# Kernel tuning notes

Measured on AMD Instinct MI355X. Metric: run time of the kernel, lower is better.

The kernel has to match this reference:

```python
import jax, jax.numpy as jnp
import numpy as np

N_NODES = 100000
N_EDGES = 1600000
DIMS = [21, 32, 64, 128, 21]  # conv1..conv4 (conv4 in-dim fixed to 128; source's 100 is a bug)


def _glorot(key, fan_in, fan_out):
    s = jnp.sqrt(6.0 / (fan_in + fan_out))
    return jax.random.uniform(key, (fan_in, fan_out), jnp.float32, -s, s)


def setup_inputs() -> dict:
    key = jax.random.key(0)
    ks = jax.random.split(key, 6)
    x = jax.random.normal(ks[0], (N_NODES, DIMS[0]), jnp.float32)
    edge_index = jax.random.randint(ks[1], (2, N_EDGES), 0, N_NODES, jnp.int64)
    inp = {"x": x, "edge_index": edge_index}
    wkeys = jax.random.split(ks[2], 4)
    for i in range(4):
        inp[f"W{i+1}"] = _glorot(wkeys[i], DIMS[i], DIMS[i + 1])
        inp[f"b{i+1}"] = jnp.zeros((DIMS[i + 1],), jnp.float32)
    return inp


def gcn_conv(x, row, col, W, b):
    # PyG GCNConv: h = x W; symmetric normalization with self loops; aggregate; + bias
    N = x.shape[0]
    h = x @ W  # [N, F]
    deg = jnp.zeros((N,), h.dtype).at[col].add(1.0) + 1.0  # +1 for self loop
    dinv = jax.lax.rsqrt(deg)
    norm = dinv[row] * dinv[col]  # [E]
    agg = jnp.zeros_like(h).at[col].add(norm[:, None] * h[row])  # scatter messages
    agg = agg + (dinv * dinv)[:, None] * h  # self-loop contribution
    return agg + b


def reference(x, edge_index, W1, b1, W2, b2, W3, b3, W4, b4):
    row, col = edge_index[0], edge_index[1]
    x = jax.nn.relu(gcn_conv(x, row, col, W1, b1))
    x = jax.nn.relu(gcn_conv(x, row, col, W2, b2))
    x = jax.nn.relu(gcn_conv(x, row, col, W3, b3))
    x = gcn_conv(x, row, col, W4, b4)
    return x
```

## Files before the change

### kernel.cpp

```cpp
#include <hip/hip_runtime.h>

#define NN 100000
#define NE 1600000
#define SH 7
#define NB_BKT 782
#define BCAP 3072
#define CSRCAP 3200
#define CHUNK 8192

static inline int cdiv(long long a, int b) { return (int)((a + b - 1) / b); }

__global__ void partition_kernel(const int* __restrict__ row, const int* __restrict__ col,
                                 int* __restrict__ bcur,
                                 unsigned int* __restrict__ packed, int E) {
    __shared__ int lh[NB_BKT];
    __shared__ int lbase[NB_BKT];
    for (int i = threadIdx.x; i < NB_BKT; i += 256) lh[i] = 0;
    __syncthreads();
    int base = blockIdx.x * CHUNK;
    int end = min(base + CHUNK, E);
    for (int e = base + threadIdx.x; e < end; e += 256) atomicAdd(&lh[col[e] >> SH], 1);
    __syncthreads();
    for (int i = threadIdx.x; i < NB_BKT; i += 256) {
        int v = lh[i];
        lbase[i] = v ? atomicAdd(&bcur[i], v) : 0;
        lh[i] = 0;
    }
    __syncthreads();
    for (int e = base + threadIdx.x; e < end; e += 256) {
        int c = col[e];
        int r = row[e];
        int b = c >> SH;
        int off = atomicAdd(&lh[b], 1);
        packed[lbase[b] + off] = ((unsigned)r << 7) | (unsigned)(c & 127);
    }
}

__global__ void bucket_nodes_place(const unsigned int* __restrict__ packed,
                                   const int* __restrict__ bcur, int* __restrict__ rowptr,
                                   int* __restrict__ rowend, float* __restrict__ dinv,
                                   int* __restrict__ csr_row, int N) {
    int b = blockIdx.x;
    __shared__ int lcnt[128];
    __shared__ int lcur[128];
    __shared__ int wt4[4];
    int t = threadIdx.x;
    if (t < 128) lcnt[t] = 0;
    __syncthreads();
    int s = b * BCAP;
    int e = bcur[b];
    for (int i = s + t; i < e; i += 256)
        atomicAdd(&lcnt[packed[i] & 127u], 1);
    __syncthreads();
    int node = (b << SH) + t;
    int v = (t < 128 && node < N) ? lcnt[t] + 1 : 0;
    int lane = t & 63, w = t >> 6;
    int incl = v;
#pragma unroll
    for (int off = 1; off < 64; off <<= 1) {
        int u = __shfl_up(incl, off, 64);
        if (lane >= off) incl += u;
    }
    if (lane == 63) wt4[w] = incl;
    __syncthreads();
    int woff = 0;
    for (int i = 0; i < w; i++) woff += wt4[i];
    int excl = woff + incl - v;
    if (t < 128 && node < N) {
        int start = b * CSRCAP + excl;
        rowptr[node] = start;
        rowend[node] = start + v;
        csr_row[start] = node;
        dinv[node] = rsqrtf((float)v);
        lcur[t] = start + 1;
    }
    __syncthreads();
    for (int i = s + t; i < e; i += 256) {
        unsigned p = packed[i];
        int r = (int)(p >> 7);
        int pos = atomicAdd(&lcur[p & 127u], 1);
        csr_row[pos] = r;
    }
}

__global__ void padx_kernel(const float* __restrict__ x, float* __restrict__ xp,
                            int* __restrict__ bcur, int N) {
    int idx = blockIdx.x * blockDim.x + threadIdx.x;
    if (idx < NB_BKT) bcur[idx] = idx * BCAP;
    if (idx >= N * 32) return;
    int n = idx >> 5;
    int k = idx & 31;
    xp[idx] = (k < 21) ? x[n * 21 + k] : 0.f;
}

template <int LPN, int FIN, int FOUT, int RJ, int OSTRIDE>
__global__ __launch_bounds__(512) void gather_gemm(
    const float4* __restrict__ h, const int* __restrict__ rowptr,
    const int* __restrict__ rowend, const int* __restrict__ csr_row,
    const float* __restrict__ dinv, const float* __restrict__ W,
    const float* __restrict__ b, float* __restrict__ out, int N) {
    constexpr int NT = 512 / LPN;
    constexpr int FINP = 4 * LPN;
    constexpr int XLD = FINP + 1;
    constexpr int JG = FOUT / RJ;
    __shared__ float xs[NT * XLD];
    __shared__ float Ws[FIN * FOUT];
    __shared__ float bs[FOUT];
    const int t = threadIdx.x;

    for (int i = t; i < FIN * FOUT; i += 512) Ws[i] = W[i];
    if (t < FOUT) bs[t] = b[t];

    const int l = t % LPN;
    const int ny = t / LPN;
    const int node = blockIdx.x * NT + ny;
    float4 acc = make_float4(0.f, 0.f, 0.f, 0.f);
    if (node < N) {
        int s = rowptr[node], e = rowend[node];
        float dn = dinv[node];
        int i = s;
        for (; i + 3 < e; i += 4) {
            int r0 = csr_row[i], r1 = csr_row[i + 1], r2 = csr_row[i + 2], r3 = csr_row[i + 3];
            float w0 = dinv[r0] * dn, w1 = dinv[r1] * dn, w2 = dinv[r2] * dn, w3 = dinv[r3] * dn;
            float4 a0 = h[(size_t)r0 * LPN + l];
            float4 a1 = h[(size_t)r1 * LPN + l];
            float4 a2 = h[(size_t)r2 * LPN + l];
            float4 a3 = h[(size_t)r3 * LPN + l];
            acc.x = fmaf(w0, a0.x, acc.x); acc.y = fmaf(w0, a0.y, acc.y);
            acc.z = fmaf(w0, a0.z, acc.z); acc.w = fmaf(w0, a0.w, acc.w);
            acc.x = fmaf(w1, a1.x, acc.x); acc.y = fmaf(w1, a1.y, acc.y);
            acc.z = fmaf(w1, a1.z, acc.z); acc.w = fmaf(w1, a1.w, acc.w);
            acc.x = fmaf(w2, a2.x, acc.x); acc.y = fmaf(w2, a2.y, acc.y);
            acc.z = fmaf(w2, a2.z, acc.z); acc.w = fmaf(w2, a2.w, acc.w);
            acc.x = fmaf(w3, a3.x, acc.x); acc.y = fmaf(w3, a3.y, acc.y);
            acc.z = fmaf(w3, a3.z, acc.z); acc.w = fmaf(w3, a3.w, acc.w);
        }
        for (; i < e; i++) {
            int r0 = csr_row[i];
            float w0 = dinv[r0] * dn;
            float4 a0 = h[(size_t)r0 * LPN + l];
            acc.x = fmaf(w0, a0.x, acc.x); acc.y = fmaf(w0, a0.y, acc.y);
            acc.z = fmaf(w0, a0.z, acc.z); acc.w = fmaf(w0, a0.w, acc.w);
        }
    }
    xs[ny * XLD + 4 * l + 0] = acc.x;
    xs[ny * XLD + 4 * l + 1] = acc.y;
    xs[ny * XLD + 4 * l + 2] = acc.z;
    xs[ny * XLD + 4 * l + 3] = acc.w;
    __syncthreads();

    const int jg = t % JG;
    const int ng = t / JG;
    float r[RJ];
#pragma unroll
    for (int jj = 0; jj < RJ; jj++) r[jj] = 0.f;
#pragma unroll 4
    for (int k = 0; k < FIN; k++) {
        float xv = xs[ng * XLD + k];
#pragma unroll
        for (int jj = 0; jj < RJ; jj++)
            r[jj] = fmaf(xv, Ws[k * FOUT + jg * RJ + jj], r[jj]);
    }
    int onode = blockIdx.x * NT + ng;
    if (onode < N) {
        float* orow = out + (size_t)onode * OSTRIDE + jg * RJ;
#pragma unroll
        for (int jj = 0; jj < RJ; jj++) r[jj] = fmaxf(r[jj] + bs[jg * RJ + jj], 0.f);
#pragma unroll
        for (int c = 0; c < RJ / 4; c++)
            *(float4*)&orow[4 * c] = make_float4(r[4 * c], r[4 * c + 1], r[4 * c + 2], r[4 * c + 3]);
    }
}

template <int LPN, bool BIAS, bool STORE21>
__global__ void gather4_kernel(const float4* __restrict__ h, const int* __restrict__ rowptr,
                               const int* __restrict__ rowend, const int* __restrict__ csr_row,
                               const float* __restrict__ dinv, const float* __restrict__ bias,
                               float* __restrict__ outp, int N) {
    int node = blockIdx.x * blockDim.y + threadIdx.y;
    if (node >= N) return;
    int l = threadIdx.x;
    int s = rowptr[node], e = rowend[node];
    float dn = dinv[node];
    float4 acc = make_float4(0.f, 0.f, 0.f, 0.f);
    int i = s;
    for (; i + 3 < e; i += 4) {
        int r0 = csr_row[i], r1 = csr_row[i + 1], r2 = csr_row[i + 2], r3 = csr_row[i + 3];
        float w0 = dinv[r0] * dn, w1 = dinv[r1] * dn, w2 = dinv[r2] * dn, w3 = dinv[r3] * dn;
        float4 a0 = h[(size_t)r0 * LPN + l];
        float4 a1 = h[(size_t)r1 * LPN + l];
        float4 a2 = h[(size_t)r2 * LPN + l];
        float4 a3 = h[(size_t)r3 * LPN + l];
        acc.x = fmaf(w0, a0.x, acc.x); acc.y = fmaf(w0, a0.y, acc.y);
        acc.z = fmaf(w0, a0.z, acc.z); acc.w = fmaf(w0, a0.w, acc.w);
        acc.x = fmaf(w1, a1.x, acc.x); acc.y = fmaf(w1, a1.y, acc.y);
        acc.z = fmaf(w1, a1.z, acc.z); acc.w = fmaf(w1, a1.w, acc.w);
        acc.x = fmaf(w2, a2.x, acc.x); acc.y = fmaf(w2, a2.y, acc.y);
        acc.z = fmaf(w2, a2.z, acc.z); acc.w = fmaf(w2, a2.w, acc.w);
        acc.x = fmaf(w3, a3.x, acc.x); acc.y = fmaf(w3, a3.y, acc.y);
        acc.z = fmaf(w3, a3.z, acc.z); acc.w = fmaf(w3, a3.w, acc.w);
    }
    for (; i < e; i++) {
        int r0 = csr_row[i];
        float w0 = dinv[r0] * dn;
        float4 a0 = h[(size_t)r0 * LPN + l];
        acc.x = fmaf(w0, a0.x, acc.x); acc.y = fmaf(w0, a0.y, acc.y);
        acc.z = fmaf(w0, a0.z, acc.z); acc.w = fmaf(w0, a0.w, acc.w);
    }
    if (STORE21) {
        int j = 4 * l;
        float v[4] = {acc.x, acc.y, acc.z, acc.w};
#pragma unroll
        for (int c = 0; c < 4; c++) {
            int jj = j + c;
            if (jj < 21) outp[(size_t)node * 21 + jj] = v[c] + (BIAS ? bias[jj] : 0.f);
        }
    } else {
        ((float4*)outp)[(size_t)node * LPN + l] = acc;
    }
}

__global__ __launch_bounds__(512, 4) void gather_gemm_l3l4(
    const float4* __restrict__ h, const int* __restrict__ rowptr,
    const int* __restrict__ rowend, const int* __restrict__ csr_row,
    const float* __restrict__ dinv, const float* __restrict__ W3,
    const float* __restrict__ b3, const float* __restrict__ W4,
    float* __restrict__ out, int N) {
    __shared__ float xs[64 * 65];
    __shared__ float4 W3v[64 * 32];
    __shared__ float4 W4v[16 * 48];
    __shared__ float b3s[128];
    const int t = threadIdx.x;
    const int node0 = blockIdx.x * 64;

    for (int sid = t; sid < 64 * 32; sid += 512) {
        int k = sid >> 5, q = sid & 31;
        int jg = q >> 2, c = q & 3;
        W3v[(k << 5) + (c << 3) + jg] = ((const float4*)W3)[sid];
    }
    for (int cid = t; cid < 16 * 48; cid += 512) {
        int i = cid / 48, rem = cid - i * 48;
        int jq = rem >> 3, jg = rem & 7;
        int k = jg * 16 + i;
        float v0 = (4 * jq + 0 < 21) ? W4[k * 21 + 4 * jq + 0] : 0.f;
        float v1 = (4 * jq + 1 < 21) ? W4[k * 21 + 4 * jq + 1] : 0.f;
        float v2 = (4 * jq + 2 < 21) ? W4[k * 21 + 4 * jq + 2] : 0.f;
        float v3 = (4 * jq + 3 < 21) ? W4[k * 21 + 4 * jq + 3] : 0.f;
        W4v[cid] = make_float4(v0, v1, v2, v3);
    }
    if (t < 128) b3s[t] = b3[t];

    {
        const int l = t & 7;
        const int ny = t >> 3;
        const int node = node0 + ny;
        float4 acc0 = make_float4(0.f, 0.f, 0.f, 0.f);
        float4 acc1 = make_float4(0.f, 0.f, 0.f, 0.f);
        if (node < N) {
            int s = rowptr[node], e = rowend[node];
            float dn = dinv[node];
            int i = s;
            for (; i + 3 < e; i += 4) {
                int r0 = csr_row[i], r1 = csr_row[i + 1];
                int r2 = csr_row[i + 2], r3 = csr_row[i + 3];
                float w0 = dinv[r0] * dn, w1 = dinv[r1] * dn;
                float w2 = dinv[r2] * dn, w3 = dinv[r3] * dn;
                const float4* p0 = h + (size_t)r0 * 16 + 2 * l;
                const float4* p1 = h + (size_t)r1 * 16 + 2 * l;
                const float4* p2 = h + (size_t)r2 * 16 + 2 * l;
                const float4* p3 = h + (size_t)r3 * 16 + 2 * l;
                float4 a0 = p0[0], c0 = p0[1];
                float4 a1 = p1[0], c1 = p1[1];
                float4 a2 = p2[0], c2 = p2[1];
                float4 a3 = p3[0], c3 = p3[1];
                acc0.x = fmaf(w0, a0.x, acc0.x); acc0.y = fmaf(w0, a0.y, acc0.y);
                acc0.z = fmaf(w0, a0.z, acc0.z); acc0.w = fmaf(w0, a0.w, acc0.w);
                acc1.x = fmaf(w0, c0.x, acc1.x); acc1.y = fmaf(w0, c0.y, acc1.y);
                acc1.z = fmaf(w0, c0.z, acc1.z); acc1.w = fmaf(w0, c0.w, acc1.w);
                acc0.x = fmaf(w1, a1.x, acc0.x); acc0.y = fmaf(w1, a1.y, acc0.y);
                acc0.z = fmaf(w1, a1.z, acc0.z); acc0.w = fmaf(w1, a1.w, acc0.w);
                acc1.x = fmaf(w1, c1.x, acc1.x); acc1.y = fmaf(w1, c1.y, acc1.y);
                acc1.z = fmaf(w1, c1.z, acc1.z); acc1.w = fmaf(w1, c1.w, acc1.w);
                acc0.x = fmaf(w2, a2.x, acc0.x); acc0.y = fmaf(w2, a2.y, acc0.y);
                acc0.z = fmaf(w2, a2.z, acc0.z); acc0.w = fmaf(w2, a2.w, acc0.w);
                acc1.x = fmaf(w2, c2.x, acc1.x); acc1.y = fmaf(w2, c2.y, acc1.y);
                acc1.z = fmaf(w2, c2.z, acc1.z); acc1.w = fmaf(w2, c2.w, acc1.w);
                acc0.x = fmaf(w3, a3.x, acc0.x); acc0.y = fmaf(w3, a3.y, acc0.y);
                acc0.z = fmaf(w3, a3.z, acc0.z); acc0.w = fmaf(w3, a3.w, acc0.w);
                acc1.x = fmaf(w3, c3.x, acc1.x); acc1.y = fmaf(w3, c3.y, acc1.y);
                acc1.z = fmaf(w3, c3.z, acc1.z); acc1.w = fmaf(w3, c3.w, acc1.w);
            }
            for (; i < e; i++) {
                int r0 = csr_row[i];
                float w0 = dinv[r0] * dn;
                const float4* p0 = h + (size_t)r0 * 16 + 2 * l;
                float4 a0 = p0[0], c0 = p0[1];
                acc0.x = fmaf(w0, a0.x, acc0.x); acc0.y = fmaf(w0, a0.y, acc0.y);
                acc0.z = fmaf(w0, a0.z, acc0.z); acc0.w = fmaf(w0, a0.w, acc0.w);
                acc1.x = fmaf(w0, c0.x, acc1.x); acc1.y = fmaf(w0, c0.y, acc1.y);
                acc1.z = fmaf(w0, c0.z, acc1.z); acc1.w = fmaf(w0, c0.w, acc1.w);
            }
        }
        float* xr = xs + ny * 65 + 8 * l;
        xr[0] = acc0.x; xr[1] = acc0.y; xr[2] = acc0.z; xr[3] = acc0.w;
        xr[4] = acc1.x; xr[5] = acc1.y; xr[6] = acc1.z; xr[7] = acc1.w;
    }
    __syncthreads();

    const int jg = t & 7;
    const int ng = t >> 3;
    const int node = node0 + ng;
    const float* arow = xs + ng * 65;

    float accA[16];
#pragma unroll
    for (int jj = 0; jj < 16; jj++) accA[jj] = 0.f;
#pragma unroll 4
    for (int k = 0; k < 64; k++) {
        float xa = arow[k];
        const float4* wb = &W3v[(k << 5) + jg];
#pragma unroll
        for (int c = 0; c < 4; c++) {
            float4 w = wb[c << 3];
            accA[4 * c + 0] = fmaf(xa, w.x, accA[4 * c + 0]);
            accA[4 * c + 1] = fmaf(xa, w.y, accA[4 * c + 1]);
            accA[4 * c + 2] = fmaf(xa, w.z, accA[4 * c + 2]);
            accA[4 * c + 3] = fmaf(xa, w.w, accA[4 * c + 3]);
        }
    }
#pragma unroll
    for (int jj = 0; jj < 16; jj++) {
        float bb = b3s[jg * 16 + jj];
        accA[jj] = fmaxf(accA[jj] + bb, 0.f);
    }

    float pA[24];
#pragma unroll
    for (int j = 0; j < 24; j++) pA[j] = 0.f;
#pragma unroll
    for (int i = 0; i < 16; i++) {
        float ha = accA[i];
        const float4* wb = &W4v[i * 48 + jg];
#pragma unroll
        for (int jq = 0; jq < 6; jq++) {
            float4 w = wb[jq << 3];
            pA[4 * jq + 0] = fmaf(ha, w.x, pA[4 * jq + 0]);
            pA[4 * jq + 1] = fmaf(ha, w.y, pA[4 * jq + 1]);
            pA[4 * jq + 2] = fmaf(ha, w.z, pA[4 * jq + 2]);
            pA[4 * jq + 3] = fmaf(ha, w.w, pA[4 * jq + 3]);
        }
    }
#pragma unroll
    for (int m = 1; m < 8; m <<= 1) {
#pragma unroll
        for (int j = 0; j < 24; j++)
            pA[j] += __shfl_xor(pA[j], m, 8);
    }
    if (node < N) {
        float* orow = out + (size_t)node * 32 + jg * 3;
        orow[0] = pA[jg * 3 + 0];
        orow[1] = pA[jg * 3 + 1];
        orow[2] = pA[jg * 3 + 2];
        if (jg < 2) *(float4*)(out + (size_t)node * 32 + 24 + 4 * jg) =
            make_float4(0.f, 0.f, 0.f, 0.f);
    }
}

extern "C" void kernel_launch(void* const* d_in, const int* in_sizes, int n_in,
                              void* d_out, int out_size, void* d_ws, size_t ws_size,
                              hipStream_t stream) {
    const float* x  = (const float*)d_in[0];
    const int*   ei = (const int*)d_in[1];
    const float* W1 = (const float*)d_in[2]; const float* b1 = (const float*)d_in[3];
    const float* W2 = (const float*)d_in[4]; const float* b2 = (const float*)d_in[5];
    const float* W3 = (const float*)d_in[6]; const float* b3 = (const float*)d_in[7];
    const float* W4 = (const float*)d_in[8]; const float* b4 = (const float*)d_in[9];
    const int* row = ei;
    const int* col = ei + NE;
    float* out = (float*)d_out;

    float* A      = (float*)d_ws;
    float* B      = A + (size_t)NN * 128;
    float* dinv   = B + (size_t)NN * 128;
    int*   rowptr = (int*)(dinv + NN);
    int*   rowend = rowptr + NN;
    int*   csr_row= rowend + NN;
    int*   bcur   = csr_row + (size_t)NB_BKT * CSRCAP;
    unsigned int* packed = (unsigned int*)A;

    const int BS = 256;
    const int NCH = cdiv(NE, CHUNK);

    padx_kernel<<<cdiv((long long)NN * 32, BS), BS, 0, stream>>>(x, B, bcur, NN);
    partition_kernel<<<NCH, 256, 0, stream>>>(row, col, bcur, packed, NE);
    bucket_nodes_place<<<NB_BKT, 256, 0, stream>>>(packed, bcur, rowptr, rowend, dinv, csr_row, NN);

    gather_gemm<8, 21, 32, 4, 32><<<cdiv(NN, 64), 512, 0, stream>>>(
        (const float4*)B, rowptr, rowend, csr_row, dinv, W1, b1, A, NN);
    gather_gemm<8, 32, 64, 8, 64><<<cdiv(NN, 64), 512, 0, stream>>>(
        (const float4*)A, rowptr, rowend, csr_row, dinv, W2, b2, B, NN);
    gather_gemm_l3l4<<<cdiv(NN, 64), 512, 0, stream>>>(
        (const float4*)B, rowptr, rowend, csr_row, dinv, W3, b3, W4, A, NN);
    {
        dim3 blk(8, 32);
        gather4_kernel<8, true, true><<<cdiv(NN, 32), blk, 0, stream>>>(
            (const float4*)A, rowptr, rowend, csr_row, dinv, b4, out, NN);
    }
}
```

Baseline: 330.8 us.

## Warp-specialize fused layer3/4 kernel into persistent gather/GEMM producer-consumer pipeline

The fused layer-3/4 kernel becomes persistent with 512 blocks looping over 32-node tiles. Half the threads gather neighbor features into a double-buffered shared tile while the other half run the two small GEMMs on the previous tile. The goal is to overlap irregular memory gathers with compute and to amortize the per-block weight staging into shared memory. In exchange, each phase gets only half the threads, and every iteration needs a block-wide barrier that couples the two halves' latencies.

```diff
diff --git a/kernel.cpp b/kernel.cpp
--- a/kernel.cpp
+++ b/kernel.cpp
@@ -7,6 +7,8 @@
 #define BCAP 3072
 #define CSRCAP 3200
 #define CHUNK 8192
+#define TILES_TOTAL 3125
+#define PIPE_BLOCKS 512
 
 static inline int cdiv(long long a, int b) { return (int)((a + b - 1) / b); }
 
@@ -220,23 +222,24 @@
     }
 }
 
-__global__ __launch_bounds__(512, 4) void gather_gemm_l3l4(
+__global__ __launch_bounds__(512, 4) void gather_gemm_l3l4_pipe(
     const float4* __restrict__ h, const int* __restrict__ rowptr,
     const int* __restrict__ rowend, const int* __restrict__ csr_row,
     const float* __restrict__ dinv, const float* __restrict__ W3,
     const float* __restrict__ b3, const float* __restrict__ W4,
     float* __restrict__ out, int N) {
-    __shared__ float xs[64 * 65];
+    __shared__ float xs[2][32 * 65];
     __shared__ float4 W3v[64 * 32];
     __shared__ float4 W4v[16 * 48];
     __shared__ float b3s[128];
     const int t = threadIdx.x;
-    const int node0 = blockIdx.x * 64;
-
-    for (int sid = t; sid < 64 * 32; sid += 512) {
-        int k = sid >> 5, q = sid & 31;
-        int jg = q >> 2, c = q & 3;
-        W3v[(k << 5) + (c << 3) + jg] = ((const float4*)W3)[sid];
+    const int b = blockIdx.x;
+
+    for (int d = t; d < 64 * 32; d += 512) {
+        int k = d >> 5;
+        int jg = d & 7;
+        int c = (d >> 3) & 3;
+        W3v[d] = ((const float4*)W3)[(k << 5) + (jg << 2) + c];
     }
     for (int cid = t; cid < 16 * 48; cid += 512) {
         int i = cid / 48, rem = cid - i * 48;
@@ -249,120 +252,129 @@
         W4v[cid] = make_float4(v0, v1, v2, v3);
     }
     if (t < 128) b3s[t] = b3[t];
-
-    {
-        const int l = t & 7;
-        const int ny = t >> 3;
-        const int node = node0 + ny;
-        float4 acc0 = make_float4(0.f, 0.f, 0.f, 0.f);
-        float4 acc1 = make_float4(0.f, 0.f, 0.f, 0.f);
-        if (node < N) {
-            int s = rowptr[node], e = rowend[node];
-            float dn = dinv[node];
-            int i = s;
-            for (; i + 3 < e; i += 4) {
-                int r0 = csr_row[i], r1 = csr_row[i + 1];
-                int r2 = csr_row[i + 2], r3 = csr_row[i + 3];
-                float w0 = dinv[r0] * dn, w1 = dinv[r1] * dn;
-                float w2 = dinv[r2] * dn, w3 = dinv[r3] * dn;
-                const float4* p0 = h + (size_t)r0 * 16 + 2 * l;
-                const float4* p1 = h + (size_t)r1 * 16 + 2 * l;
-                const float4* p2 = h + (size_t)r2 * 16 + 2 * l;
-                const float4* p3 = h + (size_t)r3 * 16 + 2 * l;
-                float4 a0 = p0[0], c0 = p0[1];
-                float4 a1 = p1[0], c1 = p1[1];
-                float4 a2 = p2[0], c2 = p2[1];
-                float4 a3 = p3[0], c3 = p3[1];
-                acc0.x = fmaf(w0, a0.x, acc0.x); acc0.y = fmaf(w0, a0.y, acc0.y);
-                acc0.z = fmaf(w0, a0.z, acc0.z); acc0.w = fmaf(w0, a0.w, acc0.w);
-                acc1.x = fmaf(w0, c0.x, acc1.x); acc1.y = fmaf(w0, c0.y, acc1.y);
-                acc1.z = fmaf(w0, c0.z, acc1.z); acc1.w = fmaf(w0, c0.w, acc1.w);
-                acc0.x = fmaf(w1, a1.x, acc0.x); acc0.y = fmaf(w1, a1.y, acc0.y);
-                acc0.z = fmaf(w1, a1.z, acc0.z); acc0.w = fmaf(w1, a1.w, acc0.w);
-                acc1.x = fmaf(w1, c1.x, acc1.x); acc1.y = fmaf(w1, c1.y, acc1.y);
-                acc1.z = fmaf(w1, c1.z, acc1.z); acc1.w = fmaf(w1, c1.w, acc1.w);
-                acc0.x = fmaf(w2, a2.x, acc0.x); acc0.y = fmaf(w2, a2.y, acc0.y);
-                acc0.z = fmaf(w2, a2.z, acc0.z); acc0.w = fmaf(w2, a2.w, acc0.w);
-                acc1.x = fmaf(w2, c2.x, acc1.x); acc1.y = fmaf(w2, c2.y, acc1.y);
-                acc1.z = fmaf(w2, c2.z, acc1.z); acc1.w = fmaf(w2, c2.w, acc1.w);
-                acc0.x = fmaf(w3, a3.x, acc0.x); acc0.y = fmaf(w3, a3.y, acc0.y);
-                acc0.z = fmaf(w3, a3.z, acc0.z); acc0.w = fmaf(w3, a3.w, acc0.w);
-                acc1.x = fmaf(w3, c3.x, acc1.x); acc1.y = fmaf(w3, c3.y, acc1.y);
-                acc1.z = fmaf(w3, c3.z, acc1.z); acc1.w = fmaf(w3, c3.w, acc1.w);
+    __syncthreads();
+
+    const int R = (TILES_TOTAL - b + PIPE_BLOCKS - 1) / PIPE_BLOCKS;
+
+    for (int r = 0; r <= R; r++) {
+        if (t < 256) {
+            if (r < R) {
+                const int l = t & 7;
+                const int ny = t >> 3;
+                const int node = (b + PIPE_BLOCKS * r) * 32 + ny;
+                float4 acc0 = make_float4(0.f, 0.f, 0.f, 0.f);
+                float4 acc1 = make_float4(0.f, 0.f, 0.f, 0.f);
+                if (node < N) {
+                    int s = rowptr[node], e = rowend[node];
+                    float dn = dinv[node];
+                    int i = s;
+                    for (; i + 3 < e; i += 4) {
+                        int r0 = csr_row[i], r1 = csr_row[i + 1];
+                        int r2 = csr_row[i + 2], r3 = csr_row[i + 3];
+                        float w0 = dinv[r0] * dn, w1 = dinv[r1] * dn;
+                        float w2 = dinv[r2] * dn, w3 = dinv[r3] * dn;
+                        const float4* p0 = h + (size_t)r0 * 16 + 2 * l;
+                        const float4* p1 = h + (size_t)r1 * 16 + 2 * l;
+                        const float4* p2 = h + (size_t)r2 * 16 + 2 * l;
+                        const float4* p3 = h + (size_t)r3 * 16 + 2 * l;
+                        float4 a0 = p0[0], c0 = p0[1];
+                        float4 a1 = p1[0], c1 = p1[1];
+                        float4 a2 = p2[0], c2 = p2[1];
+                        float4 a3 = p3[0], c3 = p3[1];
+                        acc0.x = fmaf(w0, a0.x, acc0.x); acc0.y = fmaf(w0, a0.y, acc0.y);
+                        acc0.z = fmaf(w0, a0.z, acc0.z); acc0.w = fmaf(w0, a0.w, acc0.w);
+                        acc1.x = fmaf(w0, c0.x, acc1.x); acc1.y = fmaf(w0, c0.y, acc1.y);
+                        acc1.z = fmaf(w0, c0.z, acc1.z); acc1.w = fmaf(w0, c0.w, acc1.w);
+                        acc0.x = fmaf(w1, a1.x, acc0.x); acc0.y = fmaf(w1, a1.y, acc0.y);
+                        acc0.z = fmaf(w1, a1.z, acc0.z); acc0.w = fmaf(w1, a1.w, acc0.w);
+                        acc1.x = fmaf(w1, c1.x, acc1.x); acc1.y = fmaf(w1, c1.y, acc1.y);
+                        acc1.z = fmaf(w1, c1.z, acc1.z); acc1.w = fmaf(w1, c1.w, acc1.w);
+                        acc0.x = fmaf(w2, a2.x, acc0.x); acc0.y = fmaf(w2, a2.y, acc0.y);
+                        acc0.z = fmaf(w2, a2.z, acc0.z); acc0.w = fmaf(w2, a2.w, acc0.w);
+                        acc1.x = fmaf(w2, c2.x, acc1.x); acc1.y = fmaf(w2, c2.y, acc1.y);
+                        acc1.z = fmaf(w2, c2.z, acc1.z); acc1.w = fmaf(w2, c2.w, acc1.w);
+                        acc0.x = fmaf(w3, a3.x, acc0.x); acc0.y = fmaf(w3, a3.y, acc0.y);
+                        acc0.z = fmaf(w3, a3.z, acc0.z); acc0.w = fmaf(w3, a3.w, acc0.w);
+                        acc1.x = fmaf(w3, c3.x, acc1.x); acc1.y = fmaf(w3, c3.y, acc1.y);
+                        acc1.z = fmaf(w3, c3.z, acc1.z); acc1.w = fmaf(w3, c3.w, acc1.w);
+                    }
+                    for (; i < e; i++) {
+                        int r0 = csr_row[i];
+                        float w0 = dinv[r0] * dn;
+                        const float4* p0 = h + (size_t)r0 * 16 + 2 * l;
+                        float4 a0 = p0[0], c0 = p0[1];
+                        acc0.x = fmaf(w0, a0.x, acc0.x); acc0.y = fmaf(w0, a0.y, acc0.y);
+                        acc0.z = fmaf(w0, a0.z, acc0.z); acc0.w = fmaf(w0, a0.w, acc0.w);
+                        acc1.x = fmaf(w0, c0.x, acc1.x); acc1.y = fmaf(w0, c0.y, acc1.y);
+                        acc1.z = fmaf(w0, c0.z, acc1.z); acc1.w = fmaf(w0, c0.w, acc1.w);
+                    }
+                }
+                float* xr = xs[r & 1] + ny * 65 + 8 * l;
+                xr[0] = acc0.x; xr[1] = acc0.y; xr[2] = acc0.z; xr[3] = acc0.w;
+                xr[4] = acc1.x; xr[5] = acc1.y; xr[6] = acc1.z; xr[7] = acc1.w;
             }
-            for (; i < e; i++) {
-                int r0 = csr_row[i];
-                float w0 = dinv[r0] * dn;
-                const float4* p0 = h + (size_t)r0 * 16 + 2 * l;
-                float4 a0 = p0[0], c0 = p0[1];
-                acc0.x = fmaf(w0, a0.x, acc0.x); acc0.y = fmaf(w0, a0.y, acc0.y);
-                acc0.z = fmaf(w0, a0.z, acc0.z); acc0.w = fmaf(w0, a0.w, acc0.w);
-                acc1.x = fmaf(w0, c0.x, acc1.x); acc1.y = fmaf(w0, c0.y, acc1.y);
-                acc1.z = fmaf(w0, c0.z, acc1.z); acc1.w = fmaf(w0, c0.w, acc1.w);
+        } else {
+            if (r >= 1) {
+                const int jg = t & 7;
+                const int ng = (t >> 3) & 31;
+                const int node = (b + PIPE_BLOCKS * (r - 1)) * 32 + ng;
+                const float* arow = xs[(r - 1) & 1] + ng * 65;
+
+                float accA[16];
+#pragma unroll
+                for (int jj = 0; jj < 16; jj++) accA[jj] = 0.f;
+#pragma unroll 4
+                for (int k = 0; k < 64; k++) {
+                    float xa = arow[k];
+                    const float4* wb = &W3v[(k << 5) + jg];
+#pragma unroll
+                    for (int c = 0; c < 4; c++) {
+                        float4 w = wb[c << 3];
+                        accA[4 * c + 0] = fmaf(xa, w.x, accA[4 * c + 0]);
+                        accA[4 * c + 1] = fmaf(xa, w.y, accA[4 * c + 1]);
+                        accA[4 * c + 2] = fmaf(xa, w.z, accA[4 * c + 2]);
+                        accA[4 * c + 3] = fmaf(xa, w.w, accA[4 * c + 3]);
+                    }
+                }
+#pragma unroll
+                for (int jj = 0; jj < 16; jj++) {
+                    float bb = b3s[jg * 16 + jj];
+                    accA[jj] = fmaxf(accA[jj] + bb, 0.f);
+                }
+
+                float pA[24];
+#pragma unroll
+                for (int j = 0; j < 24; j++) pA[j] = 0.f;
+#pragma unroll
+                for (int i = 0; i < 16; i++) {
+                    float ha = accA[i];
+                    const float4* wb = &W4v[i * 48 + jg];
+#pragma unroll
+                    for (int jq = 0; jq < 6; jq++) {
+                        float4 w = wb[jq << 3];
+                        pA[4 * jq + 0] = fmaf(ha, w.x, pA[4 * jq + 0]);
+                        pA[4 * jq + 1] = fmaf(ha, w.y, pA[4 * jq + 1]);
+                        pA[4 * jq + 2] = fmaf(ha, w.z, pA[4 * jq + 2]);
+                        pA[4 * jq + 3] = fmaf(ha, w.w, pA[4 * jq + 3]);
+                    }
+                }
+#pragma unroll
+                for (int m = 1; m < 8; m <<= 1) {
+#pragma unroll
+                    for (int j = 0; j < 24; j++)
+                        pA[j] += __shfl_xor(pA[j], m, 8);
+                }
+                if (node < N) {
+                    float* orow = out + (size_t)node * 32 + jg * 3;
+                    orow[0] = pA[jg * 3 + 0];
+                    orow[1] = pA[jg * 3 + 1];
+                    orow[2] = pA[jg * 3 + 2];
+                    if (jg < 2) *(float4*)(out + (size_t)node * 32 + 24 + 4 * jg) =
+                        make_float4(0.f, 0.f, 0.f, 0.f);
+                }
             }
         }
-        float* xr = xs + ny * 65 + 8 * l;
-        xr[0] = acc0.x; xr[1] = acc0.y; xr[2] = acc0.z; xr[3] = acc0.w;
-        xr[4] = acc1.x; xr[5] = acc1.y; xr[6] = acc1.z; xr[7] = acc1.w;
-    }
-    __syncthreads();
-
-    const int jg = t & 7;
-    const int ng = t >> 3;
-    const int node = node0 + ng;
-    const float* arow = xs + ng * 65;
-
-    float accA[16];
-#pragma unroll
-    for (int jj = 0; jj < 16; jj++) accA[jj] = 0.f;
-#pragma unroll 4
-    for (int k = 0; k < 64; k++) {
-        float xa = arow[k];
-        const float4* wb = &W3v[(k << 5) + jg];
-#pragma unroll
-        for (int c = 0; c < 4; c++) {
-            float4 w = wb[c << 3];
-            accA[4 * c + 0] = fmaf(xa, w.x, accA[4 * c + 0]);
-            accA[4 * c + 1] = fmaf(xa, w.y, accA[4 * c + 1]);
-            accA[4 * c + 2] = fmaf(xa, w.z, accA[4 * c + 2]);
-            accA[4 * c + 3] = fmaf(xa, w.w, accA[4 * c + 3]);
-        }
-    }
-#pragma unroll
-    for (int jj = 0; jj < 16; jj++) {
-        float bb = b3s[jg * 16 + jj];
-        accA[jj] = fmaxf(accA[jj] + bb, 0.f);
-    }
-
-    float pA[24];
-#pragma unroll
-    for (int j = 0; j < 24; j++) pA[j] = 0.f;
-#pragma unroll
-    for (int i = 0; i < 16; i++) {
-        float ha = accA[i];
-        const float4* wb = &W4v[i * 48 + jg];
-#pragma unroll
-        for (int jq = 0; jq < 6; jq++) {
-            float4 w = wb[jq << 3];
-            pA[4 * jq + 0] = fmaf(ha, w.x, pA[4 * jq + 0]);
-            pA[4 * jq + 1] = fmaf(ha, w.y, pA[4 * jq + 1]);
-            pA[4 * jq + 2] = fmaf(ha, w.z, pA[4 * jq + 2]);
-            pA[4 * jq + 3] = fmaf(ha, w.w, pA[4 * jq + 3]);
-        }
-    }
-#pragma unroll
-    for (int m = 1; m < 8; m <<= 1) {
-#pragma unroll
-        for (int j = 0; j < 24; j++)
-            pA[j] += __shfl_xor(pA[j], m, 8);
-    }
-    if (node < N) {
-        float* orow = out + (size_t)node * 32 + jg * 3;
-        orow[0] = pA[jg * 3 + 0];
-        orow[1] = pA[jg * 3 + 1];
-        orow[2] = pA[jg * 3 + 2];
-        if (jg < 2) *(float4*)(out + (size_t)node * 32 + 24 + 4 * jg) =
-            make_float4(0.f, 0.f, 0.f, 0.f);
+        __syncthreads();
     }
 }
 
@@ -399,7 +411,7 @@
         (const float4*)B, rowptr, rowend, csr_row, dinv, W1, b1, A, NN);
     gather_gemm<8, 32, 64, 8, 64><<<cdiv(NN, 64), 512, 0, stream>>>(
         (const float4*)A, rowptr, rowend, csr_row, dinv, W2, b2, B, NN);
-    gather_gemm_l3l4<<<cdiv(NN, 64), 512, 0, stream>>>(
+    gather_gemm_l3l4_pipe<<<PIPE_BLOCKS, 512, 0, stream>>>(
         (const float4*)B, rowptr, rowend, csr_row, dinv, W3, b3, W4, A, NN);
     {
         dim3 blk(8, 32);
```

After: 312.7 us. 5.5% less time.
